# Kernel tuning notes

Hardware: AMD Instinct MI355X
Metric: run time of the kernel (lower is better)

Reference implementation:

```python
import jax, jax.numpy as jnp
import numpy as np
import math

HEAD_SIZE = 64
WHERE_CONST = -10000.0


def setup_inputs() -> dict:
    key = jax.random.key(0)
    k1, k2, k3 = jax.random.split(key, 3)
    shape = (4, 16, 2048, 64)  # [B, H, S, D]
    q = jax.random.normal(k1, shape, dtype=jnp.float32)
    k = jax.random.normal(k2, shape, dtype=jnp.float32)
    v = jax.random.normal(k3, shape, dtype=jnp.float32)
    return {"q": q, "k": k, "v": v}


def reference(q, k, v):
    # scores: [B, H, Sq, Sk]
    scale = 1.0 / math.sqrt(HEAD_SIZE)
    scores = jnp.einsum('bhqd,bhkd->bhqk', q, k) * scale
    q_len, k_len = q.shape[-2], k.shape[-2]
    causal_mask = jnp.tril(jnp.ones((q_len, k_len), dtype=bool))[None, None]
    scores = jnp.where(causal_mask, scores, WHERE_CONST)
    probs = jax.nn.softmax(scores, axis=-1)
    # dropout rate is 0.0 -> identity
    out = jnp.einsum('bhqk,bhkd->bhqd', probs, v)  # [B, H, S, D]
    out = jnp.swapaxes(out, 1, 2)                  # [B, S, H, D]
    B, S, H, D = out.shape
    return out.reshape(B, S, H * D)
```

## Files before the change

### kernel.cpp

```cpp
#include <hip/hip_runtime.h>
#include <hip/hip_bf16.h>

typedef __bf16 bf16x8_t __attribute__((ext_vector_type(8)));
typedef float  f32x4_t  __attribute__((ext_vector_type(4)));
typedef short  short8_t __attribute__((ext_vector_type(8)));
typedef short  short4_t __attribute__((ext_vector_type(4)));

#define NB   4
#define NH   16
#define SEQ  2048
#define HD   64
#define BQ   64
#define BKV  64
#define LSTR 72

#define MASK2 (-14426.950408889634f)
#define QSCL  (0.18033688011112042f)

__device__ __forceinline__ int swz(int rowi, int blk) {
    return rowi * LSTR + (((blk) ^ (rowi >> 3)) & 7) * 8;
}

__global__ void __launch_bounds__(256)
fa_fwd(const float* __restrict__ qg,
       const float* __restrict__ kg,
       const float* __restrict__ vg,
       float* __restrict__ outg) {
    __shared__ alignas(16) short k_lds[BKV * LSTR];
    __shared__ alignas(16) short vt_lds[HD * LSTR];
    __shared__ alignas(16) short p_lds[BQ * LSTR];

    const int tid  = threadIdx.x;
    const int wave = tid >> 6;
    const int lane = tid & 63;
    const int l16  = lane & 15;
    const int quad = lane >> 4;

    const int bh = blockIdx.x;
    const int qt = (int)gridDim.y - 1 - (int)blockIdx.y;
    const int q0 = qt * BQ;

    const size_t base = (size_t)bh * SEQ * HD;
    const float* qp = qg + base;
    const float* kp = kg + base;
    const float* vp = vg + base;

    bf16x8_t qf0, qf1;
    {
        const float* qr = qp + (size_t)(q0 + wave * 16 + l16) * HD;
        f32x4_t qa = *(const f32x4_t*)(qr + quad * 8);
        f32x4_t qb = *(const f32x4_t*)(qr + quad * 8 + 4);
        f32x4_t qc = *(const f32x4_t*)(qr + 32 + quad * 8);
        f32x4_t qd = *(const f32x4_t*)(qr + 32 + quad * 8 + 4);
        #pragma unroll
        for (int j = 0; j < 4; ++j) {
            qf0[j]     = (__bf16)(qa[j] * QSCL);
            qf0[4 + j] = (__bf16)(qb[j] * QSCL);
            qf1[j]     = (__bf16)(qc[j] * QSCL);
            qf1[4 + j] = (__bf16)(qd[j] * QSCL);
        }
    }

    f32x4_t o_acc[4];
    const f32x4_t zero4 = {0.0f, 0.0f, 0.0f, 0.0f};
    #pragma unroll
    for (int c = 0; c < 4; ++c) o_acc[c] = zero4;
    float m_x = MASK2, l_x = 0.0f;

    const int sr = tid >> 4;
    const int cb = tid & 15;
    const int d0 = cb * 4;

    f32x4_t kreg[4], vreg[4];

    auto issue = [&](int kt0) {
        const float* kr = kp + (size_t)(kt0 + 4 * sr) * HD + d0;
        const float* vr = vp + (size_t)(kt0 + 4 * sr) * HD + d0;
        #pragma unroll
        for (int i = 0; i < 4; ++i) {
            kreg[i] = *(const f32x4_t*)(kr + i * HD);
            vreg[i] = *(const f32x4_t*)(vr + i * HD);
        }
    };

    auto stage = [&]() {
        #pragma unroll
        for (int i = 0; i < 4; ++i) {
            const int r0 = 4 * sr + i;
            short4_t kw;
            #pragma unroll
            for (int j = 0; j < 4; ++j) kw[j] = __builtin_bit_cast(short, (__bf16)kreg[i][j]);
            *(short4_t*)&k_lds[swz(r0, cb >> 1) + (cb & 1) * 4] = kw;
        }
        #pragma unroll
        for (int j = 0; j < 4; ++j) {
            short4_t vw;
            #pragma unroll
            for (int i = 0; i < 4; ++i) vw[i] = __builtin_bit_cast(short, (__bf16)vreg[i][j]);
            *(short4_t*)&vt_lds[swz(d0 + j, sr >> 1) + (sr & 1) * 4] = vw;
        }
    };

    issue(0);

    const int ntiles = qt + 1;
    for (int t = 0; t < ntiles; ++t) {
        const int kt0 = t * BKV;
        __syncthreads();
        stage();
        __syncthreads();
        if (t + 1 < ntiles) issue(kt0 + BKV);

        f32x4_t s_acc[4];
        #pragma unroll
        for (int c = 0; c < 4; ++c) s_acc[c] = zero4;
        __builtin_amdgcn_s_setprio(1);
        #pragma unroll
        for (int c = 0; c < 4; ++c) {
            const int kvrow = c * 16 + l16;
            bf16x8_t kf0 = __builtin_bit_cast(bf16x8_t, *(const short8_t*)&k_lds[swz(kvrow, quad)]);
            bf16x8_t kf1 = __builtin_bit_cast(bf16x8_t, *(const short8_t*)&k_lds[swz(kvrow, quad + 4)]);
            s_acc[c] = __builtin_amdgcn_mfma_f32_16x16x32_bf16(kf0, qf0, s_acc[c], 0, 0, 0);
            s_acc[c] = __builtin_amdgcn_mfma_f32_16x16x32_bf16(kf1, qf1, s_acc[c], 0, 0, 0);
        }
        __builtin_amdgcn_s_setprio(0);

        float sv[4][4];
        float vmax = MASK2;
        const bool diag = (kt0 == q0);
        const int qloc = wave * 16 + l16;
        #pragma unroll
        for (int c = 0; c < 4; ++c) {
            #pragma unroll
            for (int r = 0; r < 4; ++r) {
                float x = s_acc[c][r];
                if (diag && (c * 16 + quad * 4 + r > qloc)) x = MASK2;
                sv[c][r] = x;
                vmax = fmaxf(vmax, x);
            }
        }
        vmax = fmaxf(vmax, __shfl_xor(vmax, 16));
        vmax = fmaxf(vmax, __shfl_xor(vmax, 32));

        if (__any((int)(vmax > m_x))) {
            float mn = fmaxf(m_x, vmax);
            float a  = __builtin_amdgcn_exp2f(m_x - mn);
            m_x = mn;
            l_x *= a;
            float ar[4];
            #pragma unroll
            for (int r = 0; r < 4; ++r)
                ar[r] = __shfl(a, (lane & 48) | (quad * 4 + r));
            #pragma unroll
            for (int c = 0; c < 4; ++c)
                #pragma unroll
                for (int r = 0; r < 4; ++r)
                    o_acc[c][r] *= ar[r];
        }

        const int prow = wave * 16 + l16;
        float rs = 0.0f;
        #pragma unroll
        for (int c = 0; c < 4; ++c) {
            short4_t pw;
            #pragma unroll
            for (int r = 0; r < 4; ++r) {
                float p = __builtin_amdgcn_exp2f(sv[c][r] - m_x);
                rs += p;
                pw[r] = __builtin_bit_cast(short, (__bf16)p);
            }
            *(short4_t*)&p_lds[swz(prow, 2 * c + (quad >> 1)) + (quad & 1) * 4] = pw;
        }
        rs += __shfl_xor(rs, 16);
        rs += __shfl_xor(rs, 32);
        l_x += rs;


        bf16x8_t pf0 = __builtin_bit_cast(bf16x8_t, *(const short8_t*)&p_lds[swz(prow, quad)]);
        bf16x8_t pf1 = __builtin_bit_cast(bf16x8_t, *(const short8_t*)&p_lds[swz(prow, quad + 4)]);
        __builtin_amdgcn_s_setprio(1);
        #pragma unroll
        for (int c = 0; c < 4; ++c) {
            const int d = c * 16 + l16;
            bf16x8_t b0 = __builtin_bit_cast(bf16x8_t, *(const short8_t*)&vt_lds[swz(d, quad)]);
            bf16x8_t b1 = __builtin_bit_cast(bf16x8_t, *(const short8_t*)&vt_lds[swz(d, quad + 4)]);
            o_acc[c] = __builtin_amdgcn_mfma_f32_16x16x32_bf16(pf0, b0, o_acc[c], 0, 0, 0);
            o_acc[c] = __builtin_amdgcn_mfma_f32_16x16x32_bf16(pf1, b1, o_acc[c], 0, 0, 0);
        }
        __builtin_amdgcn_s_setprio(0);
    }

    const int b = bh >> 4;
    const int h = bh & 15;
    #pragma unroll
    for (int r = 0; r < 4; ++r) {
        const float lr = __shfl(l_x, (lane & 48) | (quad * 4 + r));
        const float inv_l = 1.0f / fmaxf(lr, 1e-30f);
        const int row = q0 + wave * 16 + quad * 4 + r;
        float* op = outg + ((size_t)b * SEQ + row) * (NH * HD) + h * HD;
        #pragma unroll
        for (int c = 0; c < 4; ++c) {
            float val = o_acc[c][r] * inv_l;
            unsigned bits = __builtin_bit_cast(unsigned, val);
            if ((bits & 0x7F800000u) == 0x7F800000u) val = 0.0f;
            op[c * 16 + l16] = val;
        }
    }
}

extern "C" void kernel_launch(void* const* d_in, const int* in_sizes, int n_in,
                              void* d_out, int out_size, void* d_ws, size_t ws_size,
                              hipStream_t stream) {
    const float* q = (const float*)d_in[0];
    const float* k = (const float*)d_in[1];
    const float* v = (const float*)d_in[2];
    float* out = (float*)d_out;
    dim3 grid(NB * NH, SEQ / BQ);
    fa_fwd<<<grid, 256, 0, stream>>>(q, k, v, out);
}
```

Baseline: 191.8 us.

## Process two 64-row query sub-tiles per block to reuse K/V tiles

Doubles the query tile to 128 rows: each wave now keeps two sets of Q fragments, accumulators and softmax state (A and B halves), and every staged K/V tile feeds both. This halves the number of K/V global loads and LDS staging passes per query row, which are the main non-MFMA cost. The A half skips the final diagonal tile, and each half applies its own causal mask. In exchange, register pressure roughly doubles, which may reduce occupancy, and the grid has half as many blocks with coarser causal load imbalance.

```diff
diff --git a/kernel.cpp b/kernel.cpp
--- a/kernel.cpp
+++ b/kernel.cpp
@@ -10,7 +10,7 @@
 #define NH   16
 #define SEQ  2048
 #define HD   64
-#define BQ   64
+#define BQ   128
 #define BKV  64
 #define LSTR 72
 
@@ -37,35 +37,37 @@
     const int quad = lane >> 4;
 
     const int bh = blockIdx.x;
-    const int qt = (int)gridDim.y - 1 - (int)blockIdx.y;
-    const int q0 = qt * BQ;
+    const int qb = (int)gridDim.y - 1 - (int)blockIdx.y;
+    const int q0 = qb * BQ;
 
     const size_t base = (size_t)bh * SEQ * HD;
     const float* qp = qg + base;
     const float* kp = kg + base;
     const float* vp = vg + base;
 
-    bf16x8_t qf0, qf1;
-    {
-        const float* qr = qp + (size_t)(q0 + wave * 16 + l16) * HD;
-        f32x4_t qa = *(const f32x4_t*)(qr + quad * 8);
-        f32x4_t qb = *(const f32x4_t*)(qr + quad * 8 + 4);
-        f32x4_t qc = *(const f32x4_t*)(qr + 32 + quad * 8);
-        f32x4_t qd = *(const f32x4_t*)(qr + 32 + quad * 8 + 4);
+    bf16x8_t qfA0, qfA1, qfB0, qfB1;
+    auto load_q = [&](int row, bf16x8_t& f0, bf16x8_t& f1) {
+        const float* qr = qp + (size_t)row * HD;
+        f32x4_t a0 = *(const f32x4_t*)(qr + quad * 8);
+        f32x4_t a1 = *(const f32x4_t*)(qr + quad * 8 + 4);
+        f32x4_t a2 = *(const f32x4_t*)(qr + 32 + quad * 8);
+        f32x4_t a3 = *(const f32x4_t*)(qr + 32 + quad * 8 + 4);
         #pragma unroll
         for (int j = 0; j < 4; ++j) {
-            qf0[j]     = (__bf16)(qa[j] * QSCL);
-            qf0[4 + j] = (__bf16)(qb[j] * QSCL);
-            qf1[j]     = (__bf16)(qc[j] * QSCL);
-            qf1[4 + j] = (__bf16)(qd[j] * QSCL);
-        }
-    }
-
-    f32x4_t o_acc[4];
+            f0[j]     = (__bf16)(a0[j] * QSCL);
+            f0[4 + j] = (__bf16)(a1[j] * QSCL);
+            f1[j]     = (__bf16)(a2[j] * QSCL);
+            f1[4 + j] = (__bf16)(a3[j] * QSCL);
+        }
+    };
+    load_q(q0 + wave * 16 + l16, qfA0, qfA1);
+    load_q(q0 + 64 + wave * 16 + l16, qfB0, qfB1);
+
+    f32x4_t oA[4], oB[4];
     const f32x4_t zero4 = {0.0f, 0.0f, 0.0f, 0.0f};
     #pragma unroll
-    for (int c = 0; c < 4; ++c) o_acc[c] = zero4;
-    float m_x = MASK2, l_x = 0.0f;
+    for (int c = 0; c < 4; ++c) { oA[c] = zero4; oB[c] = zero4; }
+    float mA = MASK2, lA = 0.0f, mB = MASK2, lB = 0.0f;
 
     const int sr = tid >> 4;
     const int cb = tid & 15;
@@ -101,9 +103,59 @@
         }
     };
 
+    const int qloc = wave * 16 + l16;
+
+    auto softmax_pstore = [&](const f32x4_t (&s)[4], float& m, float& l,
+                              f32x4_t (&o)[4], bool diag, int prow_) {
+        float sv[4][4];
+        float vmax = MASK2;
+        #pragma unroll
+        for (int c = 0; c < 4; ++c) {
+            #pragma unroll
+            for (int r = 0; r < 4; ++r) {
+                float x = s[c][r];
+                if (diag && (c * 16 + quad * 4 + r > qloc)) x = MASK2;
+                sv[c][r] = x;
+                vmax = fmaxf(vmax, x);
+            }
+        }
+        vmax = fmaxf(vmax, __shfl_xor(vmax, 16));
+        vmax = fmaxf(vmax, __shfl_xor(vmax, 32));
+        if (__any((int)(vmax > m))) {
+            float mn = fmaxf(m, vmax);
+            float a  = __builtin_amdgcn_exp2f(m - mn);
+            m = mn;
+            l *= a;
+            float ar[4];
+            #pragma unroll
+            for (int r = 0; r < 4; ++r)
+                ar[r] = __shfl(a, (lane & 48) | (quad * 4 + r));
+            #pragma unroll
+            for (int c = 0; c < 4; ++c)
+                #pragma unroll
+                for (int r = 0; r < 4; ++r)
+                    o[c][r] *= ar[r];
+        }
+        float rs = 0.0f;
+        #pragma unroll
+        for (int c = 0; c < 4; ++c) {
+            short4_t pw;
+            #pragma unroll
+            for (int r = 0; r < 4; ++r) {
+                float p = __builtin_amdgcn_exp2f(sv[c][r] - m);
+                rs += p;
+                pw[r] = __builtin_bit_cast(short, (__bf16)p);
+            }
+            *(short4_t*)&p_lds[swz(prow_, 2 * c + (quad >> 1)) + (quad & 1) * 4] = pw;
+        }
+        rs += __shfl_xor(rs, 16);
+        rs += __shfl_xor(rs, 32);
+        l += rs;
+    };
+
     issue(0);
 
-    const int ntiles = qt + 1;
+    const int ntiles = 2 * qb + 2;
     for (int t = 0; t < ntiles; ++t) {
         const int kt0 = t * BKV;
         __syncthreads();
@@ -111,101 +163,76 @@
         __syncthreads();
         if (t + 1 < ntiles) issue(kt0 + BKV);
 
-        f32x4_t s_acc[4];
-        #pragma unroll
-        for (int c = 0; c < 4; ++c) s_acc[c] = zero4;
+        const bool doA   = (t < ntiles - 1);
+        const bool diagA = (t == ntiles - 2);
+        const bool diagB = (t == ntiles - 1);
+
+        f32x4_t sA[4], sB[4];
+        #pragma unroll
+        for (int c = 0; c < 4; ++c) { sA[c] = zero4; sB[c] = zero4; }
         __builtin_amdgcn_s_setprio(1);
         #pragma unroll
         for (int c = 0; c < 4; ++c) {
             const int kvrow = c * 16 + l16;
             bf16x8_t kf0 = __builtin_bit_cast(bf16x8_t, *(const short8_t*)&k_lds[swz(kvrow, quad)]);
             bf16x8_t kf1 = __builtin_bit_cast(bf16x8_t, *(const short8_t*)&k_lds[swz(kvrow, quad + 4)]);
-            s_acc[c] = __builtin_amdgcn_mfma_f32_16x16x32_bf16(kf0, qf0, s_acc[c], 0, 0, 0);
-            s_acc[c] = __builtin_amdgcn_mfma_f32_16x16x32_bf16(kf1, qf1, s_acc[c], 0, 0, 0);
+            if (doA) {
+                sA[c] = __builtin_amdgcn_mfma_f32_16x16x32_bf16(kf0, qfA0, sA[c], 0, 0, 0);
+                sA[c] = __builtin_amdgcn_mfma_f32_16x16x32_bf16(kf1, qfA1, sA[c], 0, 0, 0);
+            }
+            sB[c] = __builtin_amdgcn_mfma_f32_16x16x32_bf16(kf0, qfB0, sB[c], 0, 0, 0);
+            sB[c] = __builtin_amdgcn_mfma_f32_16x16x32_bf16(kf1, qfB1, sB[c], 0, 0, 0);
         }
         __builtin_amdgcn_s_setprio(0);
 
-        float sv[4][4];
-        float vmax = MASK2;
-        const bool diag = (kt0 == q0);
-        const int qloc = wave * 16 + l16;
-        #pragma unroll
-        for (int c = 0; c < 4; ++c) {
-            #pragma unroll
-            for (int r = 0; r < 4; ++r) {
-                float x = s_acc[c][r];
-                if (diag && (c * 16 + quad * 4 + r > qloc)) x = MASK2;
-                sv[c][r] = x;
-                vmax = fmaxf(vmax, x);
-            }
-        }
-        vmax = fmaxf(vmax, __shfl_xor(vmax, 16));
-        vmax = fmaxf(vmax, __shfl_xor(vmax, 32));
-
-        if (__any((int)(vmax > m_x))) {
-            float mn = fmaxf(m_x, vmax);
-            float a  = __builtin_amdgcn_exp2f(m_x - mn);
-            m_x = mn;
-            l_x *= a;
-            float ar[4];
-            #pragma unroll
-            for (int r = 0; r < 4; ++r)
-                ar[r] = __shfl(a, (lane & 48) | (quad * 4 + r));
-            #pragma unroll
-            for (int c = 0; c < 4; ++c)
-                #pragma unroll
-                for (int r = 0; r < 4; ++r)
-                    o_acc[c][r] *= ar[r];
-        }
-
-        const int prow = wave * 16 + l16;
-        float rs = 0.0f;
-        #pragma unroll
-        for (int c = 0; c < 4; ++c) {
-            short4_t pw;
-            #pragma unroll
-            for (int r = 0; r < 4; ++r) {
-                float p = __builtin_amdgcn_exp2f(sv[c][r] - m_x);
-                rs += p;
-                pw[r] = __builtin_bit_cast(short, (__bf16)p);
-            }
-            *(short4_t*)&p_lds[swz(prow, 2 * c + (quad >> 1)) + (quad & 1) * 4] = pw;
-        }
-        rs += __shfl_xor(rs, 16);
-        rs += __shfl_xor(rs, 32);
-        l_x += rs;
-
-
-        bf16x8_t pf0 = __builtin_bit_cast(bf16x8_t, *(const short8_t*)&p_lds[swz(prow, quad)]);
-        bf16x8_t pf1 = __builtin_bit_cast(bf16x8_t, *(const short8_t*)&p_lds[swz(prow, quad + 4)]);
+        const int prowA = wave * 16 + l16;
+        if (doA) softmax_pstore(sA, mA, lA, oA, diagA, prowA);
+        softmax_pstore(sB, mB, lB, oB, diagB, 64 + prowA);
+
+
+        bf16x8_t pfA0, pfA1;
+        if (doA) {
+            pfA0 = __builtin_bit_cast(bf16x8_t, *(const short8_t*)&p_lds[swz(prowA, quad)]);
+            pfA1 = __builtin_bit_cast(bf16x8_t, *(const short8_t*)&p_lds[swz(prowA, quad + 4)]);
+        }
+        bf16x8_t pfB0 = __builtin_bit_cast(bf16x8_t, *(const short8_t*)&p_lds[swz(64 + prowA, quad)]);
+        bf16x8_t pfB1 = __builtin_bit_cast(bf16x8_t, *(const short8_t*)&p_lds[swz(64 + prowA, quad + 4)]);
         __builtin_amdgcn_s_setprio(1);
         #pragma unroll
         for (int c = 0; c < 4; ++c) {
             const int d = c * 16 + l16;
             bf16x8_t b0 = __builtin_bit_cast(bf16x8_t, *(const short8_t*)&vt_lds[swz(d, quad)]);
             bf16x8_t b1 = __builtin_bit_cast(bf16x8_t, *(const short8_t*)&vt_lds[swz(d, quad + 4)]);
-            o_acc[c] = __builtin_amdgcn_mfma_f32_16x16x32_bf16(pf0, b0, o_acc[c], 0, 0, 0);
-            o_acc[c] = __builtin_amdgcn_mfma_f32_16x16x32_bf16(pf1, b1, o_acc[c], 0, 0, 0);
+            if (doA) {
+                oA[c] = __builtin_amdgcn_mfma_f32_16x16x32_bf16(pfA0, b0, oA[c], 0, 0, 0);
+                oA[c] = __builtin_amdgcn_mfma_f32_16x16x32_bf16(pfA1, b1, oA[c], 0, 0, 0);
+            }
+            oB[c] = __builtin_amdgcn_mfma_f32_16x16x32_bf16(pfB0, b0, oB[c], 0, 0, 0);
+            oB[c] = __builtin_amdgcn_mfma_f32_16x16x32_bf16(pfB1, b1, oB[c], 0, 0, 0);
         }
         __builtin_amdgcn_s_setprio(0);
     }
 
     const int b = bh >> 4;
     const int h = bh & 15;
-    #pragma unroll
-    for (int r = 0; r < 4; ++r) {
-        const float lr = __shfl(l_x, (lane & 48) | (quad * 4 + r));
-        const float inv_l = 1.0f / fmaxf(lr, 1e-30f);
-        const int row = q0 + wave * 16 + quad * 4 + r;
-        float* op = outg + ((size_t)b * SEQ + row) * (NH * HD) + h * HD;
-        #pragma unroll
-        for (int c = 0; c < 4; ++c) {
-            float val = o_acc[c][r] * inv_l;
-            unsigned bits = __builtin_bit_cast(unsigned, val);
-            if ((bits & 0x7F800000u) == 0x7F800000u) val = 0.0f;
-            op[c * 16 + l16] = val;
-        }
-    }
+    auto store_o = [&](const f32x4_t (&o)[4], float l, int row_base) {
+        #pragma unroll
+        for (int r = 0; r < 4; ++r) {
+            const float lr = __shfl(l, (lane & 48) | (quad * 4 + r));
+            const float inv_l = 1.0f / fmaxf(lr, 1e-30f);
+            const int row = row_base + quad * 4 + r;
+            float* op = outg + ((size_t)b * SEQ + row) * (NH * HD) + h * HD;
+            #pragma unroll
+            for (int c = 0; c < 4; ++c) {
+                float val = o[c][r] * inv_l;
+                unsigned bits = __builtin_bit_cast(unsigned, val);
+                if ((bits & 0x7F800000u) == 0x7F800000u) val = 0.0f;
+                op[c * 16 + l16] = val;
+            }
+        }
+    };
+    store_o(oA, lA, q0 + wave * 16);
+    store_o(oB, lB, q0 + 64 + wave * 16);
 }
 
 extern "C" void kernel_launch(void* const* d_in, const int* in_sizes, int n_in,
```

New measurement: 199.3 us. +3.9%, slower.

## Pair complementary causal query tiles per block for balanced work

Applied to the files above, without the earlier changes.

Each block now handles two query tiles, z and NQT-1-z, one after the other, so every block does the same total number of causal KV tiles. The grid is halved. The first K/V tile of the second run is prefetched during the last iteration of the first run. This removes the tail imbalance from causal triangular work, but it halves the number of blocks and serialises the two tiles inside one block.

```diff
diff --git a/kernel.cpp b/kernel.cpp
--- a/kernel.cpp
+++ b/kernel.cpp
@@ -10,8 +10,9 @@
 #define NH   16
 #define SEQ  2048
 #define HD   64
-#define BQ   64
+#define QT   64
 #define BKV  64
+#define NQT  (SEQ / QT)
 #define LSTR 72
 
 #define MASK2 (-14426.950408889634f)
@@ -28,7 +29,7 @@
        float* __restrict__ outg) {
     __shared__ alignas(16) short k_lds[BKV * LSTR];
     __shared__ alignas(16) short vt_lds[HD * LSTR];
-    __shared__ alignas(16) short p_lds[BQ * LSTR];
+    __shared__ alignas(16) short p_lds[QT * LSTR];
 
     const int tid  = threadIdx.x;
     const int wave = tid >> 6;
@@ -37,36 +38,13 @@
     const int quad = lane >> 4;
 
     const int bh = blockIdx.x;
-    const int qt = (int)gridDim.y - 1 - (int)blockIdx.y;
-    const int q0 = qt * BQ;
+    const int z  = blockIdx.y;
 
     const size_t base = (size_t)bh * SEQ * HD;
     const float* qp = qg + base;
     const float* kp = kg + base;
     const float* vp = vg + base;
 
-    bf16x8_t qf0, qf1;
-    {
-        const float* qr = qp + (size_t)(q0 + wave * 16 + l16) * HD;
-        f32x4_t qa = *(const f32x4_t*)(qr + quad * 8);
-        f32x4_t qb = *(const f32x4_t*)(qr + quad * 8 + 4);
-        f32x4_t qc = *(const f32x4_t*)(qr + 32 + quad * 8);
-        f32x4_t qd = *(const f32x4_t*)(qr + 32 + quad * 8 + 4);
-        #pragma unroll
-        for (int j = 0; j < 4; ++j) {
-            qf0[j]     = (__bf16)(qa[j] * QSCL);
-            qf0[4 + j] = (__bf16)(qb[j] * QSCL);
-            qf1[j]     = (__bf16)(qc[j] * QSCL);
-            qf1[4 + j] = (__bf16)(qd[j] * QSCL);
-        }
-    }
-
-    f32x4_t o_acc[4];
-    const f32x4_t zero4 = {0.0f, 0.0f, 0.0f, 0.0f};
-    #pragma unroll
-    for (int c = 0; c < 4; ++c) o_acc[c] = zero4;
-    float m_x = MASK2, l_x = 0.0f;
-
     const int sr = tid >> 4;
     const int cb = tid & 15;
     const int d0 = cb * 4;
@@ -101,109 +79,140 @@
         }
     };
 
-    issue(0);
-
-    const int ntiles = qt + 1;
-    for (int t = 0; t < ntiles; ++t) {
-        const int kt0 = t * BKV;
-        __syncthreads();
-        stage();
-        __syncthreads();
-        if (t + 1 < ntiles) issue(kt0 + BKV);
-
-        f32x4_t s_acc[4];
-        #pragma unroll
-        for (int c = 0; c < 4; ++c) s_acc[c] = zero4;
-        __builtin_amdgcn_s_setprio(1);
-        #pragma unroll
-        for (int c = 0; c < 4; ++c) {
-            const int kvrow = c * 16 + l16;
-            bf16x8_t kf0 = __builtin_bit_cast(bf16x8_t, *(const short8_t*)&k_lds[swz(kvrow, quad)]);
-            bf16x8_t kf1 = __builtin_bit_cast(bf16x8_t, *(const short8_t*)&k_lds[swz(kvrow, quad + 4)]);
-            s_acc[c] = __builtin_amdgcn_mfma_f32_16x16x32_bf16(kf0, qf0, s_acc[c], 0, 0, 0);
-            s_acc[c] = __builtin_amdgcn_mfma_f32_16x16x32_bf16(kf1, qf1, s_acc[c], 0, 0, 0);
-        }
-        __builtin_amdgcn_s_setprio(0);
-
-        float sv[4][4];
-        float vmax = MASK2;
-        const bool diag = (kt0 == q0);
-        const int qloc = wave * 16 + l16;
-        #pragma unroll
-        for (int c = 0; c < 4; ++c) {
-            #pragma unroll
-            for (int r = 0; r < 4; ++r) {
-                float x = s_acc[c][r];
-                if (diag && (c * 16 + quad * 4 + r > qloc)) x = MASK2;
-                sv[c][r] = x;
-                vmax = fmaxf(vmax, x);
-            }
-        }
-        vmax = fmaxf(vmax, __shfl_xor(vmax, 16));
-        vmax = fmaxf(vmax, __shfl_xor(vmax, 32));
-
-        if (__any((int)(vmax > m_x))) {
-            float mn = fmaxf(m_x, vmax);
-            float a  = __builtin_amdgcn_exp2f(m_x - mn);
-            m_x = mn;
-            l_x *= a;
-            float ar[4];
-            #pragma unroll
-            for (int r = 0; r < 4; ++r)
-                ar[r] = __shfl(a, (lane & 48) | (quad * 4 + r));
-            #pragma unroll
-            for (int c = 0; c < 4; ++c)
-                #pragma unroll
-                for (int r = 0; r < 4; ++r)
-                    o_acc[c][r] *= ar[r];
-        }
-
-        const int prow = wave * 16 + l16;
-        float rs = 0.0f;
-        #pragma unroll
-        for (int c = 0; c < 4; ++c) {
-            short4_t pw;
-            #pragma unroll
-            for (int r = 0; r < 4; ++r) {
-                float p = __builtin_amdgcn_exp2f(sv[c][r] - m_x);
-                rs += p;
-                pw[r] = __builtin_bit_cast(short, (__bf16)p);
-            }
-            *(short4_t*)&p_lds[swz(prow, 2 * c + (quad >> 1)) + (quad & 1) * 4] = pw;
-        }
-        rs += __shfl_xor(rs, 16);
-        rs += __shfl_xor(rs, 32);
-        l_x += rs;
-
-
-        bf16x8_t pf0 = __builtin_bit_cast(bf16x8_t, *(const short8_t*)&p_lds[swz(prow, quad)]);
-        bf16x8_t pf1 = __builtin_bit_cast(bf16x8_t, *(const short8_t*)&p_lds[swz(prow, quad + 4)]);
-        __builtin_amdgcn_s_setprio(1);
-        #pragma unroll
-        for (int c = 0; c < 4; ++c) {
-            const int d = c * 16 + l16;
-            bf16x8_t b0 = __builtin_bit_cast(bf16x8_t, *(const short8_t*)&vt_lds[swz(d, quad)]);
-            bf16x8_t b1 = __builtin_bit_cast(bf16x8_t, *(const short8_t*)&vt_lds[swz(d, quad + 4)]);
-            o_acc[c] = __builtin_amdgcn_mfma_f32_16x16x32_bf16(pf0, b0, o_acc[c], 0, 0, 0);
-            o_acc[c] = __builtin_amdgcn_mfma_f32_16x16x32_bf16(pf1, b1, o_acc[c], 0, 0, 0);
-        }
-        __builtin_amdgcn_s_setprio(0);
-    }
-
+    const int qloc = wave * 16 + l16;
     const int b = bh >> 4;
     const int h = bh & 15;
-    #pragma unroll
-    for (int r = 0; r < 4; ++r) {
-        const float lr = __shfl(l_x, (lane & 48) | (quad * 4 + r));
-        const float inv_l = 1.0f / fmaxf(lr, 1e-30f);
-        const int row = q0 + wave * 16 + quad * 4 + r;
-        float* op = outg + ((size_t)b * SEQ + row) * (NH * HD) + h * HD;
-        #pragma unroll
-        for (int c = 0; c < 4; ++c) {
-            float val = o_acc[c][r] * inv_l;
-            unsigned bits = __builtin_bit_cast(unsigned, val);
-            if ((bits & 0x7F800000u) == 0x7F800000u) val = 0.0f;
-            op[c * 16 + l16] = val;
+    const f32x4_t zero4 = {0.0f, 0.0f, 0.0f, 0.0f};
+
+    issue(0);
+
+    #pragma unroll 1
+    for (int run = 0; run < 2; ++run) {
+        const int qt = (run == 0) ? (NQT - 1 - z) : z;
+        const int q0 = qt * QT;
+        const int nt = qt + 1;
+
+        bf16x8_t qf0, qf1;
+        {
+            const float* qr = qp + (size_t)(q0 + wave * 16 + l16) * HD;
+            f32x4_t a0 = *(const f32x4_t*)(qr + quad * 8);
+            f32x4_t a1 = *(const f32x4_t*)(qr + quad * 8 + 4);
+            f32x4_t a2 = *(const f32x4_t*)(qr + 32 + quad * 8);
+            f32x4_t a3 = *(const f32x4_t*)(qr + 32 + quad * 8 + 4);
+            #pragma unroll
+            for (int j = 0; j < 4; ++j) {
+                qf0[j]     = (__bf16)(a0[j] * QSCL);
+                qf0[4 + j] = (__bf16)(a1[j] * QSCL);
+                qf1[j]     = (__bf16)(a2[j] * QSCL);
+                qf1[4 + j] = (__bf16)(a3[j] * QSCL);
+            }
+        }
+
+        f32x4_t o_acc[4];
+        #pragma unroll
+        for (int c = 0; c < 4; ++c) o_acc[c] = zero4;
+        float m_x = MASK2, l_x = 0.0f;
+
+        #pragma unroll 1
+        for (int t = 0; t < nt; ++t) {
+            const int kt0 = t * BKV;
+            __syncthreads();
+            stage();
+            __syncthreads();
+            if (t + 1 < nt) issue(kt0 + BKV);
+            else if (run == 0) issue(0);
+
+            f32x4_t s_acc[4];
+            #pragma unroll
+            for (int c = 0; c < 4; ++c) s_acc[c] = zero4;
+            __builtin_amdgcn_s_setprio(1);
+            #pragma unroll
+            for (int c = 0; c < 4; ++c) {
+                const int kvrow = c * 16 + l16;
+                bf16x8_t kf0 = __builtin_bit_cast(bf16x8_t, *(const short8_t*)&k_lds[swz(kvrow, quad)]);
+                bf16x8_t kf1 = __builtin_bit_cast(bf16x8_t, *(const short8_t*)&k_lds[swz(kvrow, quad + 4)]);
+                s_acc[c] = __builtin_amdgcn_mfma_f32_16x16x32_bf16(kf0, qf0, s_acc[c], 0, 0, 0);
+                s_acc[c] = __builtin_amdgcn_mfma_f32_16x16x32_bf16(kf1, qf1, s_acc[c], 0, 0, 0);
+            }
+            __builtin_amdgcn_s_setprio(0);
+
+            float sv[4][4];
+            float vmax = MASK2;
+            const bool diag = (t == nt - 1);
+            #pragma unroll
+            for (int c = 0; c < 4; ++c) {
+                #pragma unroll
+                for (int r = 0; r < 4; ++r) {
+                    float x = s_acc[c][r];
+                    if (diag && (c * 16 + quad * 4 + r > qloc)) x = MASK2;
+                    sv[c][r] = x;
+                    vmax = fmaxf(vmax, x);
+                }
+            }
+            vmax = fmaxf(vmax, __shfl_xor(vmax, 16));
+            vmax = fmaxf(vmax, __shfl_xor(vmax, 32));
+
+            if (__any((int)(vmax > m_x))) {
+                float mn = fmaxf(m_x, vmax);
+                float a  = __builtin_amdgcn_exp2f(m_x - mn);
+                m_x = mn;
+                l_x *= a;
+                float ar[4];
+                #pragma unroll
+                for (int r = 0; r < 4; ++r)
+                    ar[r] = __shfl(a, (lane & 48) | (quad * 4 + r));
+                #pragma unroll
+                for (int c = 0; c < 4; ++c)
+                    #pragma unroll
+                    for (int r = 0; r < 4; ++r)
+                        o_acc[c][r] *= ar[r];
+            }
+
+            const int prow = wave * 16 + l16;
+            float rs = 0.0f;
+            #pragma unroll
+            for (int c = 0; c < 4; ++c) {
+                short4_t pw;
+                #pragma unroll
+                for (int r = 0; r < 4; ++r) {
+                    float p = __builtin_amdgcn_exp2f(sv[c][r] - m_x);
+                    rs += p;
+                    pw[r] = __builtin_bit_cast(short, (__bf16)p);
+                }
+                *(short4_t*)&p_lds[swz(prow, 2 * c + (quad >> 1)) + (quad & 1) * 4] = pw;
+            }
+            rs += __shfl_xor(rs, 16);
+            rs += __shfl_xor(rs, 32);
+            l_x += rs;
+
+
+            bf16x8_t pf0 = __builtin_bit_cast(bf16x8_t, *(const short8_t*)&p_lds[swz(prow, quad)]);
+            bf16x8_t pf1 = __builtin_bit_cast(bf16x8_t, *(const short8_t*)&p_lds[swz(prow, quad + 4)]);
+            __builtin_amdgcn_s_setprio(1);
+            #pragma unroll
+            for (int c = 0; c < 4; ++c) {
+                const int d = c * 16 + l16;
+                bf16x8_t b0 = __builtin_bit_cast(bf16x8_t, *(const short8_t*)&vt_lds[swz(d, quad)]);
+                bf16x8_t b1 = __builtin_bit_cast(bf16x8_t, *(const short8_t*)&vt_lds[swz(d, quad + 4)]);
+                o_acc[c] = __builtin_amdgcn_mfma_f32_16x16x32_bf16(pf0, b0, o_acc[c], 0, 0, 0);
+                o_acc[c] = __builtin_amdgcn_mfma_f32_16x16x32_bf16(pf1, b1, o_acc[c], 0, 0, 0);
+            }
+            __builtin_amdgcn_s_setprio(0);
+        }
+
+        #pragma unroll
+        for (int r = 0; r < 4; ++r) {
+            const float lr = __shfl(l_x, (lane & 48) | (quad * 4 + r));
+            const float inv_l = 1.0f / fmaxf(lr, 1e-30f);
+            const int row = q0 + wave * 16 + quad * 4 + r;
+            float* op = outg + ((size_t)b * SEQ + row) * (NH * HD) + h * HD;
+            #pragma unroll
+            for (int c = 0; c < 4; ++c) {
+                float val = o_acc[c][r] * inv_l;
+                unsigned bits = __builtin_bit_cast(unsigned, val);
+                if ((bits & 0x7F800000u) == 0x7F800000u) val = 0.0f;
+                op[c * 16 + l16] = val;
+            }
         }
     }
 }
@@ -215,6 +224,6 @@
     const float* k = (const float*)d_in[1];
     const float* v = (const float*)d_in[2];
     float* out = (float*)d_out;
-    dim3 grid(NB * NH, SEQ / BQ);
+    dim3 grid(NB * NH, NQT / 2);
     fa_fwd<<<grid, 256, 0, stream>>>(q, k, v, out);
 }
```

Measured after the change: 207.7 us. +8.3%, slower.
